# Kernel optimization log

Measured on AMD Instinct MI355X. Metric: run time of the kernel, lower is better.

The kernel has to match this reference:

```python
import jax, jax.numpy as jnp
import numpy as np

LOG_MAX = float(np.log(1000.0 / 16.0))  # dw/dh clamp from BoxCoder.decode
NMS_THRESH = 0.7


def setup_inputs() -> dict:
    key = jax.random.key(0)
    k1, k2, k3, k4, k5, k6 = jax.random.split(key, 6)
    N, B = 262144, 4
    im_h, im_w = 800, 1280
    # plausible anchors: random centers inside image, sizes in [16, 216]
    cx = jax.random.uniform(k1, (N,)) * im_w
    cy = jax.random.uniform(k2, (N,)) * im_h
    aw = jax.random.uniform(k3, (N,)) * 200.0 + 16.0
    ah = jax.random.uniform(k4, (N,)) * 200.0 + 16.0
    anchors = jnp.stack([cx - 0.5 * aw, cy - 0.5 * ah, cx + 0.5 * aw, cy + 0.5 * ah], axis=1).astype(jnp.float32)
    pred_bbox_deltas = (jax.random.normal(k5, (B, N, 4)) * 0.2).astype(jnp.float32)
    objectness = jax.random.normal(k6, (B, N)).astype(jnp.float32)
    return {
        'anchors': anchors,
        'pred_bbox_deltas': pred_bbox_deltas,
        'objectness': objectness,
        'im_h': im_h,
        'im_w': im_w,
        'post_nms_top_n': 1000,
    }


def _decode_clip(anchors, deltas, im_h, im_w):
    # BoxCoder.decode with weights (1,1,1,1), then clip to image bounds.
    aw = anchors[:, 2] - anchors[:, 0]          # [N]
    ah = anchors[:, 3] - anchors[:, 1]
    acx = anchors[:, 0] + 0.5 * aw
    acy = anchors[:, 1] + 0.5 * ah
    dx, dy = deltas[..., 0], deltas[..., 1]     # [B,N]
    dw = jnp.minimum(deltas[..., 2], LOG_MAX)
    dh = jnp.minimum(deltas[..., 3], LOG_MAX)
    pcx = dx * aw + acx
    pcy = dy * ah + acy
    pw = jnp.exp(dw) * aw
    ph = jnp.exp(dh) * ah
    x1 = jnp.clip(pcx - 0.5 * pw, 0.0, im_w)
    y1 = jnp.clip(pcy - 0.5 * ph, 0.0, im_h)
    x2 = jnp.clip(pcx + 0.5 * pw, 0.0, im_w)
    y2 = jnp.clip(pcy + 0.5 * ph, 0.0, im_h)
    return jnp.stack([x1, y1, x2, y2], axis=-1)  # [B,N,4]


def _nms_indices(boxes, scores, k):
    # Greedy NMS (torchvision semantics: suppress IoU > thresh), fixed k picks.
    bs = jax.lax.stop_gradient(boxes)           # indices are non-differentiable
    ss = jax.lax.stop_gradient(scores)
    areas = (bs[:, 2] - bs[:, 0]) * (bs[:, 3] - bs[:, 1])

    def body(cur, _):
        i = jnp.argmax(cur)
        picked = cur[i]
        bb = bs[i]
        ix1 = jnp.maximum(bb[0], bs[:, 0])
        iy1 = jnp.maximum(bb[1], bs[:, 1])
        ix2 = jnp.minimum(bb[2], bs[:, 2])
        iy2 = jnp.minimum(bb[3], bs[:, 3])
        inter = jnp.maximum(ix2 - ix1, 0.0) * jnp.maximum(iy2 - iy1, 0.0)
        barea = (bb[2] - bb[0]) * (bb[3] - bb[1])
        iou = inter / (barea + areas - inter + 1e-9)
        cur = jnp.where(iou > NMS_THRESH, -jnp.inf, cur).at[i].set(-jnp.inf)
        return cur, (i, picked)

    _, (idx, picked) = jax.lax.scan(body, ss, None, length=k)
    return idx, jnp.isfinite(picked)            # valid flags pad positions


def reference(anchors, pred_bbox_deltas, objectness, im_h, im_w, post_nms_top_n):
    boxes = _decode_clip(anchors, pred_bbox_deltas, float(im_h), float(im_w))  # [B,N,4]
    area = (boxes[..., 2] - boxes[..., 0]) * (boxes[..., 3] - boxes[..., 1])
    # area > 1 filter, expressed as score masking (keeps shapes static)
    scores = jnp.where(area > 1.0, objectness, -jnp.inf)

    idx, valid = jax.vmap(lambda b, s: _nms_indices(b, s, post_nms_top_n))(boxes, scores)
    kept_boxes = jnp.take_along_axis(boxes, idx[..., None], axis=1)   # [B,K,4]
    kept_scores = jnp.take_along_axis(scores, idx, axis=1)            # [B,K]
    vf = valid.astype(boxes.dtype)
    kept_boxes = kept_boxes * vf[..., None]
    kept_scores = jnp.where(valid, kept_scores, 0.0)
    # [B, K, 6] = (x1,y1,x2,y2,score,valid)
    return jnp.concatenate([kept_boxes, kept_scores[..., None], vf[..., None]], axis=-1)
```

## Files before the change

kernel.cpp:

```cpp
#include <hip/hip_runtime.h>
#include <cstdint>
#include <cstddef>

#define NBINS 32768
#define FINB 64u
#define CAP_C 2048
#define NW (CAP_C / 64)
#define TARGET 1792u
#define KMAX 1008
#define MROWS 16
#define HB 1024
#define HE 32768
#define CNT_STRIDE 64
#define ARRIVE_OFF 16
#define CPB 64

typedef unsigned long long u64;

__device__ __forceinline__ unsigned orderable(float f) {
  unsigned b = __float_as_uint(f);
  return (b & 0x80000000u) ? ~b : (b | 0x80000000u);
}

__device__ __forceinline__ void gload_lds16(const u64* g, u64* l) {
  __builtin_amdgcn_global_load_lds(
      (const __attribute__((address_space(1))) unsigned int*)g,
      (__attribute__((address_space(3))) unsigned int*)l, 16, 0, 0);
}

__global__ void decode_kernel(const float4* __restrict__ anchors,
                              const float4* __restrict__ deltas,
                              const float* __restrict__ obj,
                              const int* __restrict__ im_h_p,
                              const int* __restrict__ im_w_p,
                              unsigned* __restrict__ keys,
                              unsigned* __restrict__ hist,
                              unsigned* __restrict__ cnt,
                              int N, int B) {
#pragma clang fp contract(off)
  int n = blockIdx.x * blockDim.x + threadIdx.x;
  int stride = gridDim.x * blockDim.x;
  for (int j = n; j < B * NBINS; j += stride) hist[j] = 0u;
  for (int j = n; j < B * CNT_STRIDE; j += stride) cnt[j] = 0u;
  if (n >= N) return;
  float imw = (float)(*im_w_p);
  float imh = (float)(*im_h_p);
  float4 a = anchors[n];
  float aw = a.z - a.x;
  float ah = a.w - a.y;
  float acx = a.x + 0.5f * aw;
  float acy = a.y + 0.5f * ah;
  const float LOGM = 4.135166556742356f;
  for (int b = 0; b < B; ++b) {
    size_t off = (size_t)b * N + n;
    float4 d = deltas[off];
    float dw = fminf(d.z, LOGM), dh = fminf(d.w, LOGM);
    float pcx = d.x * aw + acx;
    float pcy = d.y * ah + acy;
    float pw = expf(dw) * aw;
    float ph = expf(dh) * ah;
    float x1 = fminf(fmaxf(pcx - 0.5f * pw, 0.0f), imw);
    float y1 = fminf(fmaxf(pcy - 0.5f * ph, 0.0f), imh);
    float x2 = fminf(fmaxf(pcx + 0.5f * pw, 0.0f), imw);
    float y2 = fminf(fmaxf(pcy + 0.5f * ph, 0.0f), imh);
    float area = (x2 - x1) * (y2 - y1);
    float sc = (area > 1.0f) ? obj[off] : -__builtin_inff();
    keys[off] = orderable(sc);
  }
}

__global__ void __launch_bounds__(HB) hist_kernel(const unsigned* __restrict__ keys,
                                                  unsigned* __restrict__ hist,
                                                  unsigned* __restrict__ T_lo,
                                                  unsigned* __restrict__ cnt,
                                                  int N) {
  __shared__ unsigned hl[NBINS / 2];
  int t = threadIdx.x, b = blockIdx.y;
  for (int i = t; i < NBINS / 2; i += HB) hl[i] = 0u;
  __syncthreads();
  const uint4* kb = (const uint4*)(keys + (size_t)b * N) + (size_t)blockIdx.x * (HE / 4);
  int lim = HE / 4;
  int rem4 = (N - blockIdx.x * HE) / 4;
  if (lim > rem4) lim = rem4;
  for (int i = t; i < lim; i += HB) {
    uint4 v = kb[i];
    unsigned b0 = v.x >> 17, b1 = v.y >> 17, b2 = v.z >> 17, b3 = v.w >> 17;
    atomicAdd(&hl[b0 >> 1], (b0 & 1u) ? 65536u : 1u);
    atomicAdd(&hl[b1 >> 1], (b1 & 1u) ? 65536u : 1u);
    atomicAdd(&hl[b2 >> 1], (b2 & 1u) ? 65536u : 1u);
    atomicAdd(&hl[b3 >> 1], (b3 & 1u) ? 65536u : 1u);
  }
  __syncthreads();
  unsigned* hg = hist + (size_t)b * NBINS;
  for (int i = t; i < NBINS / 2; i += HB) {
    unsigned v = hl[i];
    unsigned clo = v & 0xFFFFu, chi = v >> 16;
    if (clo) atomicAdd(&hg[2 * i], clo);
    if (chi) atomicAdd(&hg[2 * i + 1], chi);
  }
  __syncthreads();
  if (t == 0) {
    __threadfence();
    unsigned old = atomicAdd(&cnt[b * CNT_STRIDE + ARRIVE_OFF], 1u);
    hl[4096] = (old == gridDim.x - 1u) ? 1u : 0u;
  }
  __syncthreads();
  if (hl[4096] == 0u) return;
  const int BPT = NBINS / 1024;
  unsigned mysum = 0;
  for (int k = 0; k < BPT; ++k) {
    unsigned bin = (unsigned)(t * BPT + k);
    if (bin >= FINB)
      mysum += __hip_atomic_load(&hg[bin], __ATOMIC_RELAXED, __HIP_MEMORY_SCOPE_AGENT);
  }
  if (t == 0) hl[2048] = 0xFFFFFFFFu;
  hl[t] = mysum;
  __syncthreads();
  for (int d = 1; d < 1024; d <<= 1) {
    unsigned v = (t + d < 1024) ? hl[t + d] : 0u;
    __syncthreads();
    hl[t] += v;
    __syncthreads();
  }
  unsigned total = hl[0];
  unsigned target = (TARGET < total) ? TARGET : total;
  unsigned above = (t + 1 < 1024) ? hl[t + 1] : 0u;
  if (total > 0u && above < target && hl[t] >= target) {
    unsigned c = above;
    for (int k = BPT - 1; k >= 0; --k) {
      unsigned bin = (unsigned)(t * BPT + k);
      if (bin < FINB) break;
      unsigned hv = __hip_atomic_load(&hg[bin], __ATOMIC_RELAXED, __HIP_MEMORY_SCOPE_AGENT);
      c += hv;
      if (c >= target) {
        unsigned T = bin;
        if (c > CAP_C && (c - hv) > 0u) T = bin + 1u;
        hl[2048] = T;
        break;
      }
    }
  }
  __syncthreads();
  if (t == 0) T_lo[b] = (total == 0u) ? 0xFFFFFFFFu : hl[2048];
}

__global__ void __launch_bounds__(1024) compact_kernel(const unsigned* __restrict__ keys,
                                                       const unsigned* __restrict__ T_lo,
                                                       u64* __restrict__ cand,
                                                       unsigned* __restrict__ cnt, int N) {
  __shared__ u64 s_w[4096];
  __shared__ unsigned s_n, s_base;
  int b = blockIdx.y, t = threadIdx.x;
  if (t == 0) s_n = 0u;
  __syncthreads();
  unsigned T = T_lo[b];
  int slice4 = N / 4 / CPB;
  const uint4* k4 = (const uint4*)(keys + (size_t)b * N) + (size_t)blockIdx.x * slice4;
  for (int i = t; i < slice4; i += 1024) {
    uint4 v = k4[i];
    int bi = (blockIdx.x * slice4 + i) * 4;
    if ((v.x >> 17) >= T) { unsigned p = atomicAdd(&s_n, 1u); if (p < 4096u) s_w[p] = ((u64)v.x << 32) | (unsigned)(~(bi + 0)); }
    if ((v.y >> 17) >= T) { unsigned p = atomicAdd(&s_n, 1u); if (p < 4096u) s_w[p] = ((u64)v.y << 32) | (unsigned)(~(bi + 1)); }
    if ((v.z >> 17) >= T) { unsigned p = atomicAdd(&s_n, 1u); if (p < 4096u) s_w[p] = ((u64)v.z << 32) | (unsigned)(~(bi + 2)); }
    if ((v.w >> 17) >= T) { unsigned p = atomicAdd(&s_n, 1u); if (p < 4096u) s_w[p] = ((u64)v.w << 32) | (unsigned)(~(bi + 3)); }
  }
  __syncthreads();
  unsigned n = s_n < 4096u ? s_n : 4096u;
  if (t == 0) s_base = (n > 0u) ? atomicAdd(&cnt[b * CNT_STRIDE], n) : 0u;
  __syncthreads();
  unsigned gb = s_base;
  for (unsigned j = t; j < n; j += 1024) {
    unsigned p = gb + j;
    if (p < CAP_C) cand[(size_t)b * CAP_C + p] = s_w[j];
  }
}

__global__ void __launch_bounds__(1024) sort_kernel(const u64* __restrict__ cand,
                                                    const unsigned* __restrict__ cntp,
                                                    const float4* __restrict__ anchors,
                                                    const float4* __restrict__ deltas,
                                                    const int* __restrict__ im_h_p,
                                                    const int* __restrict__ im_w_p,
                                                    float4* __restrict__ sboxes,
                                                    float* __restrict__ sscore,
                                                    int N) {
#pragma clang fp contract(off)
  __shared__ u64 sk[CAP_C];
  int b = blockIdx.x, t = threadIdx.x;
  int cnt = (int)cntp[b * CNT_STRIDE];
  if (cnt > CAP_C) cnt = CAP_C;
  for (int i = t; i < CAP_C; i += 1024)
    sk[i] = (i < cnt) ? cand[(size_t)b * CAP_C + i] : 0ull;
  __syncthreads();
  for (unsigned kk = 2; kk <= CAP_C; kk <<= 1) {
    for (unsigned j = kk >> 1; j >= 1u; j >>= 1) {
      if (j >= 64u) __syncthreads();
      unsigned pid = (unsigned)t;
      unsigned i = ((pid & ~(j - 1u)) << 1) | (pid & (j - 1u));
      unsigned p = i | j;
      u64 va = sk[i], vb = sk[p];
      bool up = ((i & kk) == 0u);
      bool sw = up ? (va < vb) : (va > vb);
      if (sw) { sk[i] = vb; sk[p] = va; }
    }
  }
  __syncthreads();
  float imw = (float)(*im_w_p);
  float imh = (float)(*im_h_p);
  const float LOGM = 4.135166556742356f;
  for (int i = t; i < CAP_C; i += 1024) {
    u64 key = sk[i];
    float4 bx = make_float4(0.f, 0.f, 0.f, 0.f);
    float sc = -__builtin_inff();
    if (i < cnt) {
      unsigned idx = ~(unsigned)(key & 0xFFFFFFFFull);
      float4 a = anchors[idx];
      float4 d = deltas[(size_t)b * N + idx];
      float aw = a.z - a.x;
      float ah = a.w - a.y;
      float acx = a.x + 0.5f * aw;
      float acy = a.y + 0.5f * ah;
      float dw = fminf(d.z, LOGM), dh = fminf(d.w, LOGM);
      float pcx = d.x * aw + acx;
      float pcy = d.y * ah + acy;
      float pw = expf(dw) * aw;
      float ph = expf(dh) * ah;
      bx.x = fminf(fmaxf(pcx - 0.5f * pw, 0.0f), imw);
      bx.y = fminf(fmaxf(pcy - 0.5f * ph, 0.0f), imh);
      bx.z = fminf(fmaxf(pcx + 0.5f * pw, 0.0f), imw);
      bx.w = fminf(fmaxf(pcy + 0.5f * ph, 0.0f), imh);
      unsigned u = (unsigned)(key >> 32);
      unsigned sb2 = (u & 0x80000000u) ? (u ^ 0x80000000u) : ~u;
      sc = __uint_as_float(sb2);
    }
    sboxes[(size_t)b * CAP_C + i] = bx;
    sscore[(size_t)b * CAP_C + i] = sc;
  }
}

__global__ void __launch_bounds__(256) mask_kernel(const float4* __restrict__ sboxes,
                                                   u64* __restrict__ mask) {
#pragma clang fp contract(off)
  __shared__ float4 sb[CAP_C];
  int b = blockIdx.y, t = threadIdx.x;
  int wave = t >> 6, lane = t & 63;
  const float4* src = sboxes + (size_t)b * CAP_C;
  for (int i = t; i < CAP_C; i += 256) sb[i] = src[i];
  __syncthreads();
  for (int r = 0; r < MROWS; ++r) {
    int row = blockIdx.x * MROWS + r;
    int c0 = row >> 6;
    float4 rb = sb[row];
    float ra = (rb.z - rb.x) * (rb.w - rb.y);
    for (int chunk = wave; chunk < NW; chunk += 4) {
      if (chunk < c0) continue;
      float4 cb = sb[chunk * 64 + lane];
      float ix1 = fmaxf(rb.x, cb.x), iy1 = fmaxf(rb.y, cb.y);
      float ix2 = fminf(rb.z, cb.z), iy2 = fminf(rb.w, cb.w);
      float inter = fmaxf(ix2 - ix1, 0.0f) * fmaxf(iy2 - iy1, 0.0f);
      float ca = (cb.z - cb.x) * (cb.w - cb.y);
      float iou = inter / (ra + ca - inter + 1e-9f);
      u64 bal = __ballot(iou > 0.7f);
      if (lane == 0)
        mask[((size_t)b * CAP_C + row) * NW + chunk] = bal;
    }
  }
}

__global__ void __launch_bounds__(256, 1) walk_kernel(const u64* __restrict__ mask,
                                                      const float4* __restrict__ sboxes,
                                                      const float* __restrict__ sscore,
                                                      const unsigned* __restrict__ cntp,
                                                      float* __restrict__ out, int K) {
  __shared__ u64 s_buf[2][64 * NW];
  __shared__ int s_keep[KMAX];
  __shared__ int s_ctl[4];
  const int b = blockIdx.x;
  const int t = threadIdx.x;
  const int wave = t >> 6, lane = t & 63;
  const u64* M = mask + (size_t)b * CAP_C * NW;
  int cnt = (int)cntp[b * CNT_STRIDE];
  if (cnt > CAP_C) cnt = CAP_C;
  const u64 lane_above = (lane == 63) ? 0ull : (~0ull << (lane + 1));
  const int colp1 = ((lane & 15) * 2) + 1;

  for (int k = 0; k < 4; ++k) {
    int c = wave + 4 * k;
    gload_lds16(M + c * 128 + lane * 2, &s_buf[0][c * 128]);
  }
  if (t == 0) { s_ctl[0] = 0; s_ctl[1] = 0; s_ctl[2] = 0; }
  __syncthreads();

  u64 removed = 0ull;
  int nk = 0;
  int base = 0;
  int cur = 0;
  const int lw = lane & 31;

  for (int tt = 0; tt < CAP_C / 64; ++tt) {
    int par = tt & 1;
    if (wave != 0) {
      int nt = tt + 1;
      if (nt > CAP_C / 64 - 1) nt = CAP_C / 64 - 1;
      const u64* src = M + (size_t)nt * (64 * NW);
      u64* dst = s_buf[cur ^ 1];
      for (int k = 0; k < 6; ++k) {
        int c = (wave - 1) + 3 * k;
        if (c < 16 && colp1 >= nt)
          gload_lds16(src + c * 128 + lane * 2, dst + c * 128);
      }
    } else {
      const u64* buf = s_buf[cur];
      int tw = tt;
      u64 D = buf[(size_t)lane * NW + tw];
      unsigned rlo = __builtin_amdgcn_readlane((unsigned)(removed & 0xFFFFFFFFull), tw);
      unsigned rhi = __builtin_amdgcn_readlane((unsigned)(removed >> 32), tw);
      u64 in_rm = ((u64)rhi << 32) | (u64)rlo;
      int rem = cnt - base;
      u64 valid = (rem >= 64) ? ~0ull : ((rem <= 0) ? 0ull : ((1ull << rem) - 1ull));
      u64 pend = (~in_rm) & valid;
      u64 keep = 0ull;
      while (pend != 0ull) {
        bool cond = ((pend >> lane) & 1ull) && ((D & pend & lane_above) != 0ull);
        u64 bal = __ballot((int)cond);
        if (bal == 0ull) { keep |= pend; break; }
        int f = __builtin_ctzll(bal);
        u64 beq = (2ull << f) - 1ull;
        keep |= pend & beq;
        unsigned dlo = __builtin_amdgcn_readlane((unsigned)(D & 0xFFFFFFFFull), f);
        unsigned dhi = __builtin_amdgcn_readlane((unsigned)(D >> 32), f);
        u64 rowf = ((u64)dhi << 32) | (u64)dlo;
        pend &= ~beq;
        pend &= ~rowf;
      }
      int cap = K - nk;
      int kc = __popcll(keep);
      if (kc > cap) {
        bool mine = ((keep >> lane) & 1ull) &&
                    (__popcll(keep & ((1ull << lane) - 1ull)) < cap);
        keep = __ballot((int)mine);
        kc = cap;
      }
      if ((keep >> lane) & 1ull)
        s_keep[nk + __popcll(keep & ((1ull << lane) - 1ull))] = base + lane;
      nk += kc;
      u64 ac0 = 0, ac1 = 0, ac2 = 0, ac3 = 0;
#pragma unroll
      for (int r = 0; r < 64; r += 4) {
        u64 m0 = buf[(size_t)(r + 0) * NW + lw];
        u64 m1 = buf[(size_t)(r + 1) * NW + lw];
        u64 m2 = buf[(size_t)(r + 2) * NW + lw];
        u64 m3 = buf[(size_t)(r + 3) * NW + lw];
        ac0 |= m0 & ((u64)0 - ((keep >> (r + 0)) & 1ull));
        ac1 |= m1 & ((u64)0 - ((keep >> (r + 1)) & 1ull));
        ac2 |= m2 & ((u64)0 - ((keep >> (r + 2)) & 1ull));
        ac3 |= m3 & ((u64)0 - ((keep >> (r + 3)) & 1ull));
      }
      removed |= (ac0 | ac1) | (ac2 | ac3);
      int stop = (base + 64 >= cnt) || (nk >= K);
      if (lane == 0) { s_ctl[par] = stop; s_ctl[2] = nk; }
    }
    __syncthreads();
    if (s_ctl[par]) break;
    base += 64;
    cur ^= 1;
  }
  __syncthreads();
  int nkf = s_ctl[2];
  for (int j = t; j < nkf; j += 256) {
    int i = s_keep[j];
    float4 bx = sboxes[(size_t)b * CAP_C + i];
    float sc = sscore[(size_t)b * CAP_C + i];
    float* row = out + ((size_t)b * K + j) * 6;
    row[0] = bx.x; row[1] = bx.y; row[2] = bx.z; row[3] = bx.w;
    row[4] = sc; row[5] = 1.0f;
  }
  for (int j = nkf + t; j < K; j += 256) {
    float* row = out + ((size_t)b * K + j) * 6;
    row[0] = 0.f; row[1] = 0.f; row[2] = 0.f; row[3] = 0.f;
    row[4] = 0.f; row[5] = 0.f;
  }
}

extern "C" void kernel_launch(void* const* d_in, const int* in_sizes, int n_in,
                              void* d_out, int out_size, void* d_ws, size_t ws_size,
                              hipStream_t stream) {
  const float4* anchors = (const float4*)d_in[0];
  const float4* deltas = (const float4*)d_in[1];
  const float* obj = (const float*)d_in[2];
  const int* imh = (const int*)d_in[3];
  const int* imw = (const int*)d_in[4];
  int N = in_sizes[0] / 4;
  int B = in_sizes[2] / N;
  int K = out_size / (B * 6);
  if (K > KMAX) K = KMAX;

  char* ws = (char*)d_ws;
  size_t off = 0;
  float4* sboxes = (float4*)(ws + off);           off += (size_t)B * CAP_C * 16;
  u64* mask = (u64*)(ws + off);                   off += (size_t)B * CAP_C * NW * 8;
  u64* cand = (u64*)(ws + off);                   off += (size_t)B * CAP_C * 8;
  unsigned* keys = (unsigned*)(ws + off);         off += (size_t)B * N * 4;
  unsigned* hist = (unsigned*)(ws + off);         off += (size_t)B * NBINS * 4;
  float* sscore = (float*)(ws + off);             off += (size_t)B * CAP_C * 4;
  unsigned* T_lo = (unsigned*)(ws + off);         off += (size_t)B * 4;
  off = (off + 255) & ~(size_t)255;
  unsigned* cnt = (unsigned*)(ws + off);          off += (size_t)B * CNT_STRIDE * 4;
  float* out = (float*)d_out;

  int nb = (N + 255) / 256;
  int P = (N + HE - 1) / HE;
  decode_kernel<<<nb, 256, 0, stream>>>(anchors, deltas, obj, imh, imw,
                                        keys, hist, cnt, N, B);
  hist_kernel<<<dim3(P, B), HB, 0, stream>>>(keys, hist, T_lo, cnt, N);
  compact_kernel<<<dim3(CPB, B), 1024, 0, stream>>>(keys, T_lo, cand, cnt, N);
  sort_kernel<<<B, 1024, 0, stream>>>(cand, cnt, anchors, deltas, imh, imw,
                                      sboxes, sscore, N);
  mask_kernel<<<dim3(CAP_C / MROWS, B), 256, 0, stream>>>(sboxes, mask);
  walk_kernel<<<B, 256, 0, stream>>>(mask, sboxes, sscore, cnt, out, K);
}
```

Measured before the change: 178.0 us.

## Fuse sort, mask and walk into one persistent kernel with flag-based handoff

Replaces the three tail kernels (sort, IoU mask, greedy walk) with a single kernel of B*32 blocks. The first B blocks sort and decode, then publish a per-batch flag; every block waits on that flag and computes a 64-row mask stripe, publishing per-stripe flags; the first B blocks then walk the mask, prefetching each stripe as soon as its flag is set. This removes two kernel launch boundaries and lets the walk overlap with mask computation. The cost is spin-waiting, which relies on all 128 blocks being co-resident to avoid deadlock, and on flags in the cnt buffer being reset between calls.

```diff
diff --git a/kernel.cpp b/kernel.cpp
--- a/kernel.cpp
+++ b/kernel.cpp
@@ -6,13 +6,15 @@
 #define FINB 64u
 #define CAP_C 2048
 #define NW (CAP_C / 64)
+#define NT (CAP_C / 64)
 #define TARGET 1792u
 #define KMAX 1008
-#define MROWS 16
 #define HB 1024
 #define HE 32768
 #define CNT_STRIDE 64
 #define ARRIVE_OFF 16
+#define SORTF_OFF 17
+#define ROWF_OFF 24
 #define CPB 64
 
 typedef unsigned long long u64;
@@ -175,210 +177,222 @@
   }
 }
 
-__global__ void __launch_bounds__(1024) sort_kernel(const u64* __restrict__ cand,
-                                                    const unsigned* __restrict__ cntp,
-                                                    const float4* __restrict__ anchors,
-                                                    const float4* __restrict__ deltas,
-                                                    const int* __restrict__ im_h_p,
-                                                    const int* __restrict__ im_w_p,
-                                                    float4* __restrict__ sboxes,
-                                                    float* __restrict__ sscore,
-                                                    int N) {
+__global__ void __launch_bounds__(1024, 1) tail_kernel(
+    const u64* __restrict__ cand, unsigned* __restrict__ cntp,
+    const float4* __restrict__ anchors, const float4* __restrict__ deltas,
+    const int* __restrict__ im_h_p, const int* __restrict__ im_w_p,
+    float4* __restrict__ sboxes, float* __restrict__ sscore,
+    u64* __restrict__ maskbuf, float* __restrict__ out,
+    int N, int B, int K) {
 #pragma clang fp contract(off)
-  __shared__ u64 sk[CAP_C];
-  int b = blockIdx.x, t = threadIdx.x;
-  int cnt = (int)cntp[b * CNT_STRIDE];
-  if (cnt > CAP_C) cnt = CAP_C;
-  for (int i = t; i < CAP_C; i += 1024)
-    sk[i] = (i < cnt) ? cand[(size_t)b * CAP_C + i] : 0ull;
-  __syncthreads();
-  for (unsigned kk = 2; kk <= CAP_C; kk <<= 1) {
-    for (unsigned j = kk >> 1; j >= 1u; j >>= 1) {
-      if (j >= 64u) __syncthreads();
-      unsigned pid = (unsigned)t;
-      unsigned i = ((pid & ~(j - 1u)) << 1) | (pid & (j - 1u));
-      unsigned p = i | j;
-      u64 va = sk[i], vb = sk[p];
-      bool up = ((i & kk) == 0u);
-      bool sw = up ? (va < vb) : (va > vb);
-      if (sw) { sk[i] = vb; sk[p] = va; }
-    }
-  }
-  __syncthreads();
-  float imw = (float)(*im_w_p);
-  float imh = (float)(*im_h_p);
-  const float LOGM = 4.135166556742356f;
-  for (int i = t; i < CAP_C; i += 1024) {
-    u64 key = sk[i];
-    float4 bx = make_float4(0.f, 0.f, 0.f, 0.f);
-    float sc = -__builtin_inff();
-    if (i < cnt) {
-      unsigned idx = ~(unsigned)(key & 0xFFFFFFFFull);
-      float4 a = anchors[idx];
-      float4 d = deltas[(size_t)b * N + idx];
-      float aw = a.z - a.x;
-      float ah = a.w - a.y;
-      float acx = a.x + 0.5f * aw;
-      float acy = a.y + 0.5f * ah;
-      float dw = fminf(d.z, LOGM), dh = fminf(d.w, LOGM);
-      float pcx = d.x * aw + acx;
-      float pcy = d.y * ah + acy;
-      float pw = expf(dw) * aw;
-      float ph = expf(dh) * ah;
-      bx.x = fminf(fmaxf(pcx - 0.5f * pw, 0.0f), imw);
-      bx.y = fminf(fmaxf(pcy - 0.5f * ph, 0.0f), imh);
-      bx.z = fminf(fmaxf(pcx + 0.5f * pw, 0.0f), imw);
-      bx.w = fminf(fmaxf(pcy + 0.5f * ph, 0.0f), imh);
-      unsigned u = (unsigned)(key >> 32);
-      unsigned sb2 = (u & 0x80000000u) ? (u ^ 0x80000000u) : ~u;
-      sc = __uint_as_float(sb2);
-    }
-    sboxes[(size_t)b * CAP_C + i] = bx;
-    sscore[(size_t)b * CAP_C + i] = sc;
-  }
-}
-
-__global__ void __launch_bounds__(256) mask_kernel(const float4* __restrict__ sboxes,
-                                                   u64* __restrict__ mask) {
-#pragma clang fp contract(off)
-  __shared__ float4 sb[CAP_C];
-  int b = blockIdx.y, t = threadIdx.x;
-  int wave = t >> 6, lane = t & 63;
-  const float4* src = sboxes + (size_t)b * CAP_C;
-  for (int i = t; i < CAP_C; i += 256) sb[i] = src[i];
-  __syncthreads();
-  for (int r = 0; r < MROWS; ++r) {
-    int row = blockIdx.x * MROWS + r;
-    int c0 = row >> 6;
-    float4 rb = sb[row];
-    float ra = (rb.z - rb.x) * (rb.w - rb.y);
-    for (int chunk = wave; chunk < NW; chunk += 4) {
-      if (chunk < c0) continue;
-      float4 cb = sb[chunk * 64 + lane];
-      float ix1 = fmaxf(rb.x, cb.x), iy1 = fmaxf(rb.y, cb.y);
-      float ix2 = fminf(rb.z, cb.z), iy2 = fminf(rb.w, cb.w);
-      float inter = fmaxf(ix2 - ix1, 0.0f) * fmaxf(iy2 - iy1, 0.0f);
-      float ca = (cb.z - cb.x) * (cb.w - cb.y);
-      float iou = inter / (ra + ca - inter + 1e-9f);
-      u64 bal = __ballot(iou > 0.7f);
-      if (lane == 0)
-        mask[((size_t)b * CAP_C + row) * NW + chunk] = bal;
-    }
-  }
-}
-
-__global__ void __launch_bounds__(256, 1) walk_kernel(const u64* __restrict__ mask,
-                                                      const float4* __restrict__ sboxes,
-                                                      const float* __restrict__ sscore,
-                                                      const unsigned* __restrict__ cntp,
-                                                      float* __restrict__ out, int K) {
-  __shared__ u64 s_buf[2][64 * NW];
-  __shared__ int s_keep[KMAX];
-  __shared__ int s_ctl[4];
-  const int b = blockIdx.x;
-  const int t = threadIdx.x;
+  __shared__ __align__(16) char smem[2 * 64 * NW * 8 + KMAX * 4 + 16];
+  u64* sk = (u64*)smem;
+  float4* sb = (float4*)smem;
+  u64(*wbuf)[64 * NW] = (u64(*)[64 * NW])smem;
+  int* s_keep = (int*)(smem + 2 * 64 * NW * 8);
+  int* s_ctl = (int*)(smem + 2 * 64 * NW * 8 + KMAX * 4);
+
+  const int bid = blockIdx.x, t = threadIdx.x;
   const int wave = t >> 6, lane = t & 63;
-  const u64* M = mask + (size_t)b * CAP_C * NW;
-  int cnt = (int)cntp[b * CNT_STRIDE];
-  if (cnt > CAP_C) cnt = CAP_C;
-  const u64 lane_above = (lane == 63) ? 0ull : (~0ull << (lane + 1));
-  const int colp1 = ((lane & 15) * 2) + 1;
-
-  for (int k = 0; k < 4; ++k) {
-    int c = wave + 4 * k;
-    gload_lds16(M + c * 128 + lane * 2, &s_buf[0][c * 128]);
-  }
-  if (t == 0) { s_ctl[0] = 0; s_ctl[1] = 0; s_ctl[2] = 0; }
-  __syncthreads();
-
-  u64 removed = 0ull;
-  int nk = 0;
-  int base = 0;
-  int cur = 0;
-  const int lw = lane & 31;
-
-  for (int tt = 0; tt < CAP_C / 64; ++tt) {
-    int par = tt & 1;
-    if (wave != 0) {
-      int nt = tt + 1;
-      if (nt > CAP_C / 64 - 1) nt = CAP_C / 64 - 1;
-      const u64* src = M + (size_t)nt * (64 * NW);
-      u64* dst = s_buf[cur ^ 1];
-      for (int k = 0; k < 6; ++k) {
-        int c = (wave - 1) + 3 * k;
-        if (c < 16 && colp1 >= nt)
+
+  if (bid < B) {
+    const int b = bid;
+    int cnt = (int)cntp[b * CNT_STRIDE];
+    if (cnt > CAP_C) cnt = CAP_C;
+    for (int i = t; i < CAP_C; i += 1024)
+      sk[i] = (i < cnt) ? cand[(size_t)b * CAP_C + i] : 0ull;
+    __syncthreads();
+    for (unsigned kk = 2; kk <= CAP_C; kk <<= 1) {
+      for (unsigned j = kk >> 1; j >= 1u; j >>= 1) {
+        if (j >= 64u) __syncthreads();
+        unsigned pid = (unsigned)t;
+        unsigned i = ((pid & ~(j - 1u)) << 1) | (pid & (j - 1u));
+        unsigned p = i | j;
+        u64 va = sk[i], vb = sk[p];
+        bool up = ((i & kk) == 0u);
+        bool sw = up ? (va < vb) : (va > vb);
+        if (sw) { sk[i] = vb; sk[p] = va; }
+      }
+    }
+    __syncthreads();
+    float imw = (float)(*im_w_p);
+    float imh = (float)(*im_h_p);
+    const float LOGM = 4.135166556742356f;
+    for (int i = t; i < CAP_C; i += 1024) {
+      u64 key = sk[i];
+      float4 bx = make_float4(0.f, 0.f, 0.f, 0.f);
+      float sc = -__builtin_inff();
+      if (i < cnt) {
+        unsigned idx = ~(unsigned)(key & 0xFFFFFFFFull);
+        float4 a = anchors[idx];
+        float4 d = deltas[(size_t)b * N + idx];
+        float aw = a.z - a.x;
+        float ah = a.w - a.y;
+        float acx = a.x + 0.5f * aw;
+        float acy = a.y + 0.5f * ah;
+        float dw = fminf(d.z, LOGM), dh = fminf(d.w, LOGM);
+        float pcx = d.x * aw + acx;
+        float pcy = d.y * ah + acy;
+        float pw = expf(dw) * aw;
+        float ph = expf(dh) * ah;
+        bx.x = fminf(fmaxf(pcx - 0.5f * pw, 0.0f), imw);
+        bx.y = fminf(fmaxf(pcy - 0.5f * ph, 0.0f), imh);
+        bx.z = fminf(fmaxf(pcx + 0.5f * pw, 0.0f), imw);
+        bx.w = fminf(fmaxf(pcy + 0.5f * ph, 0.0f), imh);
+        unsigned u = (unsigned)(key >> 32);
+        unsigned sb2 = (u & 0x80000000u) ? (u ^ 0x80000000u) : ~u;
+        sc = __uint_as_float(sb2);
+      }
+      sboxes[(size_t)b * CAP_C + i] = bx;
+      sscore[(size_t)b * CAP_C + i] = sc;
+    }
+    __syncthreads();
+    if (t == 0) {
+      __threadfence();
+      __hip_atomic_store(&cntp[b * CNT_STRIDE + SORTF_OFF], 1u,
+                         __ATOMIC_RELEASE, __HIP_MEMORY_SCOPE_AGENT);
+    }
+  }
+
+  const int mb = bid >> 5, mj = bid & 31;
+  while (__hip_atomic_load(&cntp[mb * CNT_STRIDE + SORTF_OFF], __ATOMIC_ACQUIRE,
+                           __HIP_MEMORY_SCOPE_AGENT) == 0u)
+    __builtin_amdgcn_s_sleep(8);
+  {
+    const float4* srcb = sboxes + (size_t)mb * CAP_C;
+    for (int i = t; i < CAP_C; i += 1024) sb[i] = srcb[i];
+    __syncthreads();
+    u64* Mm = maskbuf + (size_t)mb * CAP_C * NW;
+    for (int g = 0; g < 4; ++g) {
+      int row = mj * 64 + wave + (g << 4);
+      float4 rb = sb[row];
+      float ra = (rb.z - rb.x) * (rb.w - rb.y);
+      for (int chunk = mj; chunk < NW; ++chunk) {
+        float4 cb = sb[chunk * 64 + lane];
+        float ix1 = fmaxf(rb.x, cb.x), iy1 = fmaxf(rb.y, cb.y);
+        float ix2 = fminf(rb.z, cb.z), iy2 = fminf(rb.w, cb.w);
+        float inter = fmaxf(ix2 - ix1, 0.0f) * fmaxf(iy2 - iy1, 0.0f);
+        float ca = (cb.z - cb.x) * (cb.w - cb.y);
+        float iou = inter / (ra + ca - inter + 1e-9f);
+        u64 bal = __ballot(iou > 0.7f);
+        if (lane == 0) Mm[(size_t)row * NW + chunk] = bal;
+      }
+    }
+    __syncthreads();
+    if (t == 0) {
+      __threadfence();
+      __hip_atomic_store(&cntp[mb * CNT_STRIDE + ROWF_OFF + mj], 1u,
+                         __ATOMIC_RELEASE, __HIP_MEMORY_SCOPE_AGENT);
+    }
+  }
+  if (bid >= B) return;
+
+  {
+    const int b = bid;
+    const u64* M = maskbuf + (size_t)b * CAP_C * NW;
+    unsigned* rowflags = &cntp[b * CNT_STRIDE + ROWF_OFF];
+    int cnt = (int)cntp[b * CNT_STRIDE];
+    if (cnt > CAP_C) cnt = CAP_C;
+    const u64 lane_above = (lane == 63) ? 0ull : (~0ull << (lane + 1));
+    const int colp1 = ((lane & 15) * 2) + 1;
+    const int lw = lane & 31;
+
+    while (__hip_atomic_load(&rowflags[0], __ATOMIC_ACQUIRE,
+                             __HIP_MEMORY_SCOPE_AGENT) == 0u)
+      __builtin_amdgcn_s_sleep(8);
+    gload_lds16(M + wave * 128 + lane * 2, &wbuf[0][wave * 128]);
+    if (t == 0) { s_ctl[0] = 0; s_ctl[1] = 0; s_ctl[2] = 0; }
+    __syncthreads();
+
+    u64 removed = 0ull;
+    int nk = 0, base = 0, cur = 0;
+
+    for (int tt = 0; tt < NT; ++tt) {
+      int par = tt & 1;
+      if (wave != 0) {
+        int nt2 = tt + 1;
+        if (nt2 > NT - 1) nt2 = NT - 1;
+        while (__hip_atomic_load(&rowflags[nt2], __ATOMIC_ACQUIRE,
+                                 __HIP_MEMORY_SCOPE_AGENT) == 0u)
+          __builtin_amdgcn_s_sleep(1);
+        const u64* src = M + (size_t)nt2 * (64 * NW);
+        u64* dst = wbuf[cur ^ 1];
+        int c = wave - 1;
+        if (colp1 >= nt2) gload_lds16(src + c * 128 + lane * 2, dst + c * 128);
+        c = wave + 14;
+        if (c < 16 && colp1 >= nt2)
           gload_lds16(src + c * 128 + lane * 2, dst + c * 128);
+      } else {
+        const u64* buf = wbuf[cur];
+        int tw = tt;
+        u64 D = buf[(size_t)lane * NW + tw];
+        unsigned rlo = __builtin_amdgcn_readlane((unsigned)(removed & 0xFFFFFFFFull), tw);
+        unsigned rhi = __builtin_amdgcn_readlane((unsigned)(removed >> 32), tw);
+        u64 in_rm = ((u64)rhi << 32) | (u64)rlo;
+        int rem = cnt - base;
+        u64 valid = (rem >= 64) ? ~0ull : ((rem <= 0) ? 0ull : ((1ull << rem) - 1ull));
+        u64 pend = (~in_rm) & valid;
+        u64 keep = 0ull;
+        while (pend != 0ull) {
+          bool cond = ((pend >> lane) & 1ull) && ((D & pend & lane_above) != 0ull);
+          u64 bal = __ballot((int)cond);
+          if (bal == 0ull) { keep |= pend; break; }
+          int f = __builtin_ctzll(bal);
+          u64 beq = (2ull << f) - 1ull;
+          keep |= pend & beq;
+          unsigned dlo = __builtin_amdgcn_readlane((unsigned)(D & 0xFFFFFFFFull), f);
+          unsigned dhi = __builtin_amdgcn_readlane((unsigned)(D >> 32), f);
+          u64 rowf = ((u64)dhi << 32) | (u64)dlo;
+          pend &= ~beq;
+          pend &= ~rowf;
+        }
+        int cap = K - nk;
+        int kc = __popcll(keep);
+        if (kc > cap) {
+          bool mine = ((keep >> lane) & 1ull) &&
+                      (__popcll(keep & ((1ull << lane) - 1ull)) < cap);
+          keep = __ballot((int)mine);
+          kc = cap;
+        }
+        if ((keep >> lane) & 1ull)
+          s_keep[nk + __popcll(keep & ((1ull << lane) - 1ull))] = base + lane;
+        nk += kc;
+        u64 ac0 = 0, ac1 = 0, ac2 = 0, ac3 = 0;
+#pragma unroll
+        for (int r = 0; r < 64; r += 4) {
+          u64 m0 = buf[(size_t)(r + 0) * NW + lw];
+          u64 m1 = buf[(size_t)(r + 1) * NW + lw];
+          u64 m2 = buf[(size_t)(r + 2) * NW + lw];
+          u64 m3 = buf[(size_t)(r + 3) * NW + lw];
+          ac0 |= m0 & ((u64)0 - ((keep >> (r + 0)) & 1ull));
+          ac1 |= m1 & ((u64)0 - ((keep >> (r + 1)) & 1ull));
+          ac2 |= m2 & ((u64)0 - ((keep >> (r + 2)) & 1ull));
+          ac3 |= m3 & ((u64)0 - ((keep >> (r + 3)) & 1ull));
+        }
+        removed |= (ac0 | ac1) | (ac2 | ac3);
+        int stop = (base + 64 >= cnt) || (nk >= K);
+        if (lane == 0) { s_ctl[par] = stop; s_ctl[2] = nk; }
       }
-    } else {
-      const u64* buf = s_buf[cur];
-      int tw = tt;
-      u64 D = buf[(size_t)lane * NW + tw];
-      unsigned rlo = __builtin_amdgcn_readlane((unsigned)(removed & 0xFFFFFFFFull), tw);
-      unsigned rhi = __builtin_amdgcn_readlane((unsigned)(removed >> 32), tw);
-      u64 in_rm = ((u64)rhi << 32) | (u64)rlo;
-      int rem = cnt - base;
-      u64 valid = (rem >= 64) ? ~0ull : ((rem <= 0) ? 0ull : ((1ull << rem) - 1ull));
-      u64 pend = (~in_rm) & valid;
-      u64 keep = 0ull;
-      while (pend != 0ull) {
-        bool cond = ((pend >> lane) & 1ull) && ((D & pend & lane_above) != 0ull);
-        u64 bal = __ballot((int)cond);
-        if (bal == 0ull) { keep |= pend; break; }
-        int f = __builtin_ctzll(bal);
-        u64 beq = (2ull << f) - 1ull;
-        keep |= pend & beq;
-        unsigned dlo = __builtin_amdgcn_readlane((unsigned)(D & 0xFFFFFFFFull), f);
-        unsigned dhi = __builtin_amdgcn_readlane((unsigned)(D >> 32), f);
-        u64 rowf = ((u64)dhi << 32) | (u64)dlo;
-        pend &= ~beq;
-        pend &= ~rowf;
-      }
-      int cap = K - nk;
-      int kc = __popcll(keep);
-      if (kc > cap) {
-        bool mine = ((keep >> lane) & 1ull) &&
-                    (__popcll(keep & ((1ull << lane) - 1ull)) < cap);
-        keep = __ballot((int)mine);
-        kc = cap;
-      }
-      if ((keep >> lane) & 1ull)
-        s_keep[nk + __popcll(keep & ((1ull << lane) - 1ull))] = base + lane;
-      nk += kc;
-      u64 ac0 = 0, ac1 = 0, ac2 = 0, ac3 = 0;
-#pragma unroll
-      for (int r = 0; r < 64; r += 4) {
-        u64 m0 = buf[(size_t)(r + 0) * NW + lw];
-        u64 m1 = buf[(size_t)(r + 1) * NW + lw];
-        u64 m2 = buf[(size_t)(r + 2) * NW + lw];
-        u64 m3 = buf[(size_t)(r + 3) * NW + lw];
-        ac0 |= m0 & ((u64)0 - ((keep >> (r + 0)) & 1ull));
-        ac1 |= m1 & ((u64)0 - ((keep >> (r + 1)) & 1ull));
-        ac2 |= m2 & ((u64)0 - ((keep >> (r + 2)) & 1ull));
-        ac3 |= m3 & ((u64)0 - ((keep >> (r + 3)) & 1ull));
-      }
-      removed |= (ac0 | ac1) | (ac2 | ac3);
-      int stop = (base + 64 >= cnt) || (nk >= K);
-      if (lane == 0) { s_ctl[par] = stop; s_ctl[2] = nk; }
-    }
-    __syncthreads();
-    if (s_ctl[par]) break;
-    base += 64;
-    cur ^= 1;
-  }
-  __syncthreads();
-  int nkf = s_ctl[2];
-  for (int j = t; j < nkf; j += 256) {
-    int i = s_keep[j];
-    float4 bx = sboxes[(size_t)b * CAP_C + i];
-    float sc = sscore[(size_t)b * CAP_C + i];
-    float* row = out + ((size_t)b * K + j) * 6;
-    row[0] = bx.x; row[1] = bx.y; row[2] = bx.z; row[3] = bx.w;
-    row[4] = sc; row[5] = 1.0f;
-  }
-  for (int j = nkf + t; j < K; j += 256) {
-    float* row = out + ((size_t)b * K + j) * 6;
-    row[0] = 0.f; row[1] = 0.f; row[2] = 0.f; row[3] = 0.f;
-    row[4] = 0.f; row[5] = 0.f;
+      __syncthreads();
+      if (s_ctl[par]) break;
+      base += 64;
+      cur ^= 1;
+    }
+    __syncthreads();
+    int nkf = s_ctl[2];
+    for (int j = t; j < nkf; j += 1024) {
+      int i = s_keep[j];
+      float4 bx = sboxes[(size_t)b * CAP_C + i];
+      float sc = sscore[(size_t)b * CAP_C + i];
+      float* row = out + ((size_t)b * K + j) * 6;
+      row[0] = bx.x; row[1] = bx.y; row[2] = bx.z; row[3] = bx.w;
+      row[4] = sc; row[5] = 1.0f;
+    }
+    for (int j = nkf + t; j < K; j += 1024) {
+      float* row = out + ((size_t)b * K + j) * 6;
+      row[0] = 0.f; row[1] = 0.f; row[2] = 0.f; row[3] = 0.f;
+      row[4] = 0.f; row[5] = 0.f;
+    }
   }
 }
 
@@ -414,8 +428,6 @@
                                         keys, hist, cnt, N, B);
   hist_kernel<<<dim3(P, B), HB, 0, stream>>>(keys, hist, T_lo, cnt, N);
   compact_kernel<<<dim3(CPB, B), 1024, 0, stream>>>(keys, T_lo, cand, cnt, N);
-  sort_kernel<<<B, 1024, 0, stream>>>(cand, cnt, anchors, deltas, imh, imw,
-                                      sboxes, sscore, N);
-  mask_kernel<<<dim3(CAP_C / MROWS, B), 256, 0, stream>>>(sboxes, mask);
-  walk_kernel<<<B, 256, 0, stream>>>(mask, sboxes, sscore, cnt, out, K);
-}
+  tail_kernel<<<B * 32, 1024, 0, stream>>>(cand, cnt, anchors, deltas, imh, imw,
+                                           sboxes, sscore, mask, out, N, B, K);
+}
```

Result: slower. 268.0 us (+50.5%).
